# Kernel optimization log

Hardware: AMD Instinct MI355X
Metric: run time of the kernel (lower is better)

Reference implementation:

```python
import jax, jax.numpy as jnp
import numpy as np
from jax import lax


def _conv(x, w, padding):
    # NCHW input, OIHW weights, stride 1, no bias
    return lax.conv_general_dilated(x, w, (1, 1), padding,
                                    dimension_numbers=('NCHW', 'OIHW', 'NCHW'))


def setup_inputs() -> dict:
    key = jax.random.key(0)
    ks = jax.random.split(key, 6)
    B, C, H, W = 16, 512, 40, 40
    return {
        'exemplar': jax.random.normal(ks[0], (B, C, H, W), jnp.float32),
        'query':    jax.random.normal(ks[1], (B, C, H, W), jnp.float32),
        'w_e':  jax.random.normal(ks[2], (256, C, 1, 1), jnp.float32) * 0.01,
        'w_q':  jax.random.normal(ks[3], (256, C, 1, 1), jnp.float32) * 0.01,
        'w_c1': jax.random.normal(ks[4], (C, C, 3, 3), jnp.float32) * 0.01,
        'w_c2': jax.random.normal(ks[5], (C, C, 3, 3), jnp.float32) * 0.01,
    }


def reference(exemplar, query, w_e, w_q, w_c1, w_c2):
    B, C, H, W = query.shape
    N = H * W
    # 1x1 projections to 256-dim correlation space
    q_corr = _conv(query, w_q, 'VALID').reshape(B, -1, N)     # [B,256,N]
    e_corr = _conv(exemplar, w_e, 'VALID').reshape(B, -1, N)  # [B,256,N]
    # A[b, n_exemplar, m_query] = <e_corr[:, n], q_corr[:, m]>
    A = jnp.einsum('bcn,bcm->bnm', e_corr, q_corr)            # [B,N,N]
    # A1 = softmax over exemplar axis, then transpose (torch: softmax(A,dim=1).T)
    A1 = jnp.swapaxes(jax.nn.softmax(A, axis=1), 1, 2)        # [B,N,N]
    # Bm = softmax(A^T, dim=1).T  == softmax(A, axis=2)
    Bm = jnp.swapaxes(jax.nn.softmax(jnp.swapaxes(A, 1, 2), axis=1), 1, 2)
    e_flat = exemplar.reshape(B, C, N)
    q_flat = query.reshape(B, C, N)
    query_att = jnp.matmul(e_flat, A1)   # [B,C,N]
    exemplar_att = jnp.matmul(q_flat, Bm)  # [B,C,N]
    input1_att = _conv(exemplar_att.reshape(B, C, H, W), w_c1, 'SAME')
    input2_att = _conv(query_att.reshape(B, C, H, W), w_c2, 'SAME')
    return jnp.concatenate([input1_att, input2_att], axis=1)  # [B,2C,H,W]
```

## Files before the change

### kernel.cpp

```cpp
#include <hip/hip_runtime.h>

typedef unsigned short u16;
typedef __attribute__((ext_vector_type(8))) short bf16x8;
typedef __attribute__((ext_vector_type(4))) float f32x4;

__device__ __forceinline__ u16 f2bf(float f) {
  union { float f; unsigned u; } v; v.f = f;
  unsigned u = v.u;
  u += 0x7fffu + ((u >> 16) & 1u);
  return (u16)(u >> 16);
}

__device__ __forceinline__ void gll16(const void* g, void* l) {
  __builtin_amdgcn_global_load_lds(
      (const __attribute__((address_space(1))) void*)g,
      (__attribute__((address_space(3))) void*)l, 16, 0, 0);
}

__global__ __launch_bounds__(256) void transp_cast_x2(const float* __restrict__ ex,
                                                      const float* __restrict__ qu,
                                                      u16* __restrict__ xte,
                                                      u16* __restrict__ xtq) {
  __shared__ float t[32][33];
  int z = blockIdx.z;
  int b = z & 15;
  const float* xb = (z < 16 ? ex : qu) + (size_t)b * 819200;
  u16* xtb = (z < 16 ? xte : xtq) + (size_t)b * 819200;
  int n0 = blockIdx.x * 32, c0 = blockIdx.y * 32;
  int tx = threadIdx.x & 31, ty = threadIdx.x >> 5;
#pragma unroll
  for (int k = 0; k < 4; k++) {
    int c = ty + k * 8;
    t[c][tx] = xb[(size_t)(c0 + c) * 1600 + n0 + tx];
  }
  __syncthreads();
#pragma unroll
  for (int k = 0; k < 4; k++) {
    int n = ty + k * 8;
    xtb[(size_t)(n0 + n) * 512 + c0 + tx] = f2bf(t[tx][n]);
  }
}

__global__ void cast_w(const float* __restrict__ we, const float* __restrict__ wq,
                       u16* __restrict__ oe, u16* __restrict__ oq) {
  int i = blockIdx.x * 256 + threadIdx.x;
  oe[i] = f2bf(we[i]);
  oq[i] = f2bf(wq[i]);
}

__global__ void repack_wc(const float* __restrict__ w1, const float* __restrict__ w2,
                          u16* __restrict__ o1, u16* __restrict__ o2) {
  const float* w = blockIdx.y ? w2 : w1;
  u16* wr = blockIdx.y ? o2 : o1;
  int idx = blockIdx.x * 256 + threadIdx.x;
  int o = idx / 4608;
  int r = idx - o * 4608;
  int t = r >> 9;
  int c = r & 511;
  wr[idx] = f2bf(w[o * 4608 + c * 9 + t]);
}

__global__ void zero_pad(u16* __restrict__ att, float* __restrict__ Z) {
  int q = blockIdx.x;
  uint4 zz; zz.x = 0; zz.y = 0; zz.z = 0; zz.w = 0;
  if (q < 32) {
    uint4* base = (uint4*)(att + (size_t)q * 903168);
    for (int i = threadIdx.x; i < 10496; i += 256) {
      int t = i >> 6, c = i & 63;
      int y, x;
      if (t < 42) { y = 0; x = t; }
      else if (t < 84) { y = 41; x = t - 42; }
      else if (t < 124) { y = 1 + (t - 84); x = 0; }
      else { y = 1 + (t - 124); x = 41; }
      base[(y * 42 + x) * 64 + c] = zz;
    }
  } else {
    uint4* p = (uint4*)Z;
    for (int i = threadIdx.x; i < 12800; i += 256) p[i] = zz;
  }
}


__global__ __launch_bounds__(256, 2) void corr_gemm128(
    const u16* __restrict__ X1, const u16* __restrict__ Wg1, u16* __restrict__ C1,
    const u16* __restrict__ X2, const u16* __restrict__ Wg2, u16* __restrict__ C2) {
  __shared__ u16 ldsA[16384];
  __shared__ u16 ldsB[16384];
  int tid = threadIdx.x;
  int flat = blockIdx.x + blockIdx.y * 13 + blockIdx.z * 26;
  int wrk = (flat & 7) * 104 + (flat >> 3);
  int z = wrk / 26;
  int r2 = wrk - z * 26;
  int by = r2 / 13, bx = r2 - by * 13;
  int b = z & 15;
  const u16* A = (z < 16 ? X1 : X2) + (size_t)b * 819200;
  const u16* B = (z < 16 ? Wg1 : Wg2);
  u16* Cb = (z < 16 ? C1 : C2) + (size_t)b * 409600;
  int m0 = bx * 128, n0 = by * 128;

  int rl = tid >> 2;
  int cs = (tid & 3) ^ ((rl >> 1) & 3);
  int ra0 = m0 + rl; ra0 = ra0 < 1600 ? ra0 : 1599;
  int ra1 = m0 + 64 + rl; ra1 = ra1 < 1600 ? ra1 : 1599;
  const char* pA0 = (const char*)(A + (size_t)ra0 * 512) + cs * 16;
  const char* pA1 = (const char*)(A + (size_t)ra1 * 512) + cs * 16;
  const char* pB0 = (const char*)(B + (size_t)(n0 + rl) * 512) + cs * 16;
  const char* pB1 = (const char*)(B + (size_t)(n0 + 64 + rl) * 512) + cs * 16;

  char* ldsAb = (char*)ldsA;
  char* ldsBb = (char*)ldsB;
  int dstT = tid * 16;

#define STAGE_U(d, kh, ks)                                              \
  {                                                                     \
    int ko = (ks) * 64;                                                 \
    int ro = ((d) * 2 + (kh)) * 8192;                                   \
    gll16(pA0 + ko, ldsAb + ro + dstT);                                 \
    gll16(pA1 + ko, ldsAb + ro + 4096 + dstT);                          \
    gll16(pB0 + ko, ldsBb + ro + dstT);                                 \
    gll16(pB1 + ko, ldsBb + ro + 4096 + dstT);                          \
  }

  int wid = tid >> 6, lane = tid & 63;
  int wm = wid & 1, wn = wid >> 1;
  int lrow = lane & 15, lquad = lane >> 4;
  int csel = (lquad ^ ((lrow >> 1) & 3)) << 4;
  int aBase = (wm * 64 + lrow) * 64 + csel;
  int bBase = (wn * 64 + lrow) * 64 + csel;

  const f32x4 fzero = {0.f, 0.f, 0.f, 0.f};
  f32x4 acc[4][4];
#pragma unroll
  for (int mi = 0; mi < 4; mi++)
#pragma unroll
    for (int ni = 0; ni < 4; ni++) acc[mi][ni] = fzero;

  bf16x8 fa0, fa1, fa2, fa3, fb0, fb1, fb2, fb3;
  bf16x8 ga0, ga1, ga2, ga3, gb0, gb1, gb2, gb3;

#define RD(pre, d, kh)                                                  \
  {                                                                     \
    const char* ra_ = ldsAb + ((d) * 2 + (kh)) * 8192 + aBase;          \
    const char* rb_ = ldsBb + ((d) * 2 + (kh)) * 8192 + bBase;          \
    pre##a0 = *(const bf16x8*)(ra_);                                    \
    pre##a1 = *(const bf16x8*)(ra_ + 1024);                             \
    pre##a2 = *(const bf16x8*)(ra_ + 2048);                             \
    pre##a3 = *(const bf16x8*)(ra_ + 3072);                             \
    pre##b0 = *(const bf16x8*)(rb_);                                    \
    pre##b1 = *(const bf16x8*)(rb_ + 1024);                             \
    pre##b2 = *(const bf16x8*)(rb_ + 2048);                             \
    pre##b3 = *(const bf16x8*)(rb_ + 3072);                             \
  }

#define MROW(mi, av, pre)                                                               \
  acc[mi][0] = __builtin_amdgcn_mfma_f32_16x16x32_bf16(av, pre##b0, acc[mi][0], 0, 0, 0); \
  acc[mi][1] = __builtin_amdgcn_mfma_f32_16x16x32_bf16(av, pre##b1, acc[mi][1], 0, 0, 0); \
  acc[mi][2] = __builtin_amdgcn_mfma_f32_16x16x32_bf16(av, pre##b2, acc[mi][2], 0, 0, 0); \
  acc[mi][3] = __builtin_amdgcn_mfma_f32_16x16x32_bf16(av, pre##b3, acc[mi][3], 0, 0, 0);

#define MALL(pre)                                                              \
  MROW(0, pre##a0, pre) MROW(1, pre##a1, pre) MROW(2, pre##a2, pre) MROW(3, pre##a3, pre)

#define PHASE(rd_d, rd_kh, rdp, cp, STG)                                       \
  {                                                                            \
    STG;                                                                       \
    asm volatile("s_waitcnt vmcnt(4)" ::: "memory");                           \
    __builtin_amdgcn_s_barrier();                                              \
    RD(rdp, rd_d, rd_kh);                                                      \
    __builtin_amdgcn_s_setprio(1);                                             \
    MALL(cp)                                                                   \
    __builtin_amdgcn_s_setprio(0);                                             \
  }

  STAGE_U(0, 0, 0);
  STAGE_U(0, 1, 1);
  asm volatile("s_waitcnt vmcnt(4)" ::: "memory");
  __builtin_amdgcn_s_barrier();
  RD(f, 0, 0);

#pragma unroll 1
  for (int it = 0; it < 4; ++it) {
    int k2 = it * 4 + 2, k3 = it * 4 + 3;
    int k4 = it * 4 + 4; k4 = k4 < 16 ? k4 : 15;
    int k5 = it * 4 + 5; k5 = k5 < 16 ? k5 : 15;
    PHASE(0, 1, g, f, STAGE_U(1, 0, k2));
    PHASE(1, 0, f, g, STAGE_U(1, 1, k3));
    PHASE(1, 1, g, f, STAGE_U(0, 0, k4));
    PHASE(0, 0, f, g, STAGE_U(0, 1, k5));
  }

#undef PHASE
#undef MALL
#undef MROW
#undef RD
#undef STAGE_U

#pragma unroll
  for (int mi = 0; mi < 4; mi++) {
#pragma unroll
    for (int r = 0; r < 4; r++) {
      int i = m0 + wm * 64 + mi * 16 + lquad * 4 + r;
      if (i >= 1600) continue;
#pragma unroll
      for (int ni = 0; ni < 4; ni++) {
        int j = n0 + wn * 64 + ni * 16 + lrow;
        Cb[(size_t)i * 256 + j] = f2bf(acc[mi][ni][r]);
      }
    }
  }
}

__global__ __launch_bounds__(256, 2) void corr_exp128(
    const u16* __restrict__ A, const u16* __restrict__ B, u16* __restrict__ E,
    u16* __restrict__ ET, float* __restrict__ Zrow, float* __restrict__ Zcol) {
  __shared__ u16 ldsA[16384];
  __shared__ u16 ldsB[16384];
  int tid = threadIdx.x;
  int flat = blockIdx.x + blockIdx.y * 13 + blockIdx.z * 169;
  int wrk = (flat & 7) * 338 + (flat >> 3);
  int b = wrk / 169;
  int r2 = wrk - b * 169;
  int by = r2 / 13, bx = r2 - by * 13;
  const u16* Ab = A + (size_t)b * 409600;
  const u16* Bb = B + (size_t)b * 409600;
  u16* Eb = E + (size_t)b * 2560000;
  u16* ETb = ET + (size_t)b * 2560000;
  int m0 = bx * 128, n0 = by * 128;

  int rl = tid >> 2;
  int cs = (tid & 3) ^ ((rl >> 1) & 3);
  int ra0 = m0 + rl; ra0 = ra0 < 1600 ? ra0 : 1599;
  int ra1 = m0 + 64 + rl; ra1 = ra1 < 1600 ? ra1 : 1599;
  int rb0 = n0 + rl; rb0 = rb0 < 1600 ? rb0 : 1599;
  int rb1 = n0 + 64 + rl; rb1 = rb1 < 1600 ? rb1 : 1599;
  const char* pA0 = (const char*)(Ab + (size_t)ra0 * 256) + cs * 16;
  const char* pA1 = (const char*)(Ab + (size_t)ra1 * 256) + cs * 16;
  const char* pB0 = (const char*)(Bb + (size_t)rb0 * 256) + cs * 16;
  const char* pB1 = (const char*)(Bb + (size_t)rb1 * 256) + cs * 16;

  char* ldsAb = (char*)ldsA;
  char* ldsBb = (char*)ldsB;
  int dstT = tid * 16;

#define STAGE_U(d, kh, ks)                                              \
  {                                                                     \
    int ko = (ks) * 64;                                                 \
    int ro = ((d) * 2 + (kh)) * 8192;                                   \
    gll16(pA0 + ko, ldsAb + ro + dstT);                                 \
    gll16(pA1 + ko, ldsAb + ro + 4096 + dstT);                          \
    gll16(pB0 + ko, ldsBb + ro + dstT);                                 \
    gll16(pB1 + ko, ldsBb + ro + 4096 + dstT);                          \
  }

  int wid = tid >> 6, lane = tid & 63;
  int wm = wid & 1, wn = wid >> 1;
  int lrow = lane & 15, lquad = lane >> 4;
  int csel = (lquad ^ ((lrow >> 1) & 3)) << 4;
  int aBase = (wm * 64 + lrow) * 64 + csel;
  int bBase = (wn * 64 + lrow) * 64 + csel;

  const f32x4 fzero = {0.f, 0.f, 0.f, 0.f};
  f32x4 acc[4][4];
#pragma unroll
  for (int mi = 0; mi < 4; mi++)
#pragma unroll
    for (int ni = 0; ni < 4; ni++) acc[mi][ni] = fzero;

  bf16x8 fa0, fa1, fa2, fa3, fb0, fb1, fb2, fb3;
  bf16x8 ga0, ga1, ga2, ga3, gb0, gb1, gb2, gb3;

#define RD(pre, d, kh)                                                  \
  {                                                                     \
    const char* ra_ = ldsAb + ((d) * 2 + (kh)) * 8192 + aBase;          \
    const char* rb_ = ldsBb + ((d) * 2 + (kh)) * 8192 + bBase;          \
    pre##a0 = *(const bf16x8*)(ra_);                                    \
    pre##a1 = *(const bf16x8*)(ra_ + 1024);                             \
    pre##a2 = *(const bf16x8*)(ra_ + 2048);                             \
    pre##a3 = *(const bf16x8*)(ra_ + 3072);                             \
    pre##b0 = *(const bf16x8*)(rb_);                                    \
    pre##b1 = *(const bf16x8*)(rb_ + 1024);                             \
    pre##b2 = *(const bf16x8*)(rb_ + 2048);                             \
    pre##b3 = *(const bf16x8*)(rb_ + 3072);                             \
  }

#define MROW(mi, av, pre)                                                               \
  acc[mi][0] = __builtin_amdgcn_mfma_f32_16x16x32_bf16(av, pre##b0, acc[mi][0], 0, 0, 0); \
  acc[mi][1] = __builtin_amdgcn_mfma_f32_16x16x32_bf16(av, pre##b1, acc[mi][1], 0, 0, 0); \
  acc[mi][2] = __builtin_amdgcn_mfma_f32_16x16x32_bf16(av, pre##b2, acc[mi][2], 0, 0, 0); \
  acc[mi][3] = __builtin_amdgcn_mfma_f32_16x16x32_bf16(av, pre##b3, acc[mi][3], 0, 0, 0);

#define MALL(pre)                                                              \
  MROW(0, pre##a0, pre) MROW(1, pre##a1, pre) MROW(2, pre##a2, pre) MROW(3, pre##a3, pre)

#define PHASE(rd_d, rd_kh, rdp, cp, STG)                                       \
  {                                                                            \
    STG;                                                                       \
    asm volatile("s_waitcnt vmcnt(4)" ::: "memory");                           \
    __builtin_amdgcn_s_barrier();                                              \
    RD(rdp, rd_d, rd_kh);                                                      \
    __builtin_amdgcn_s_setprio(1);                                             \
    MALL(cp)                                                                   \
    __builtin_amdgcn_s_setprio(0);                                             \
  }

  STAGE_U(0, 0, 0);
  STAGE_U(0, 1, 1);
  asm volatile("s_waitcnt vmcnt(4)" ::: "memory");
  __builtin_amdgcn_s_barrier();
  RD(f, 0, 0);

#pragma unroll 1
  for (int it = 0; it < 2; ++it) {
    int k2 = it * 4 + 2, k3 = it * 4 + 3;
    int k4 = it * 4 + 4; k4 = k4 < 8 ? k4 : 7;
    int k5 = it * 4 + 5; k5 = k5 < 8 ? k5 : 7;
    PHASE(0, 1, g, f, STAGE_U(1, 0, k2));
    PHASE(1, 0, f, g, STAGE_U(1, 1, k3));
    PHASE(1, 1, g, f, STAGE_U(0, 0, k4));
    PHASE(0, 0, f, g, STAGE_U(0, 1, k5));
  }

#undef PHASE
#undef MALL
#undef MROW
#undef RD
#undef STAGE_U

  __syncthreads();

  const int TS = 136;
  u16* T = ldsA;
  float colacc[4] = {0.f, 0.f, 0.f, 0.f};
#pragma unroll
  for (int s = 0; s < 4; s++) {
    if (wm == (s >> 1)) {
      int smi0 = (s & 1) * 2;
#pragma unroll
      for (int mi2 = 0; mi2 < 2; mi2++) {
        int mi = smi0 + mi2;
        float rowp[4] = {0.f, 0.f, 0.f, 0.f};
#pragma unroll
        for (int ni = 0; ni < 4; ni++) {
          int j = n0 + wn * 64 + ni * 16 + lrow;
          bool jv = j < 1600;
#pragma unroll
          for (int r = 0; r < 4; r++) {
            int i = m0 + wm * 64 + mi * 16 + lquad * 4 + r;
            float e = __expf(acc[mi][ni][r]);
            T[(mi2 * 16 + lquad * 4 + r) * TS + wn * 64 + ni * 16 + lrow] = f2bf(e);
            rowp[r] += jv ? e : 0.f;
            colacc[ni] += (i < 1600) ? e : 0.f;
          }
        }
#pragma unroll
        for (int r = 0; r < 4; r++) {
          float v = rowp[r];
          v += __shfl_xor(v, 1);
          v += __shfl_xor(v, 2);
          v += __shfl_xor(v, 4);
          v += __shfl_xor(v, 8);
          int i = m0 + wm * 64 + mi * 16 + lquad * 4 + r;
          if (lrow == 0 && i < 1600) atomicAdd(&Zrow[b * 1600 + i], v);
        }
      }
    }
    __syncthreads();
#pragma unroll
    for (int p = 0; p < 2; p++) {
      int jj = tid + p * 256;
      int ml = jj >> 4, n8 = jj & 15;
      int gi = m0 + s * 32 + ml, gj = n0 + n8 * 8;
      if (gi < 1600 && gj < 1600)
        *(uint4*)(Eb + (size_t)gi * 1600 + gj) = *(const uint4*)&T[ml * TS + n8 * 8];
    }
#pragma unroll
    for (int p = 0; p < 4; p++) {
      int jj = tid + p * 256;
      int n = jj >> 3, m4 = jj & 7;
      int gm = m0 + s * 32 + m4 * 4, gn = n0 + n;
      if (gn < 1600 && gm < 1600) {
        ushort4 v;
        v.x = T[(m4 * 4 + 0) * TS + n];
        v.y = T[(m4 * 4 + 1) * TS + n];
        v.z = T[(m4 * 4 + 2) * TS + n];
        v.w = T[(m4 * 4 + 3) * TS + n];
        *(ushort4*)(ETb + (size_t)gn * 1600 + gm) = v;
      }
    }
    __syncthreads();
  }
#pragma unroll
  for (int ni = 0; ni < 4; ni++) {
    float v = colacc[ni];
    v += __shfl_xor(v, 16);
    v += __shfl_xor(v, 32);
    int j = n0 + wn * 64 + ni * 16 + lrow;
    if (lquad == 0 && j < 1600) atomicAdd(&Zcol[b * 1600 + j], v);
  }
}

__global__ void scale_div(const float* __restrict__ ex, const float* __restrict__ qu,
                          const float* __restrict__ Zcol, const float* __restrict__ Zrow,
                          u16* __restrict__ ebf, u16* __restrict__ qbf) {
  const float* x; const float* Z; u16* o;
  if (blockIdx.y == 0) { x = ex; Z = Zcol; o = ebf; }
  else { x = qu; Z = Zrow; o = qbf; }
  size_t idx = (size_t)blockIdx.x * 256 + threadIdx.x;
  int b = (int)(idx / 819200);
  int i = (int)(idx % 1600);
  o[idx] = f2bf(x[idx] / Z[b * 1600 + i]);
}

__global__ __launch_bounds__(256, 2) void att_gemm128(
    const u16* __restrict__ Aw1, const u16* __restrict__ Bp1, u16* __restrict__ C1,
    const u16* __restrict__ Aw2, const u16* __restrict__ Bp2, u16* __restrict__ C2) {
  __shared__ u16 ldsA[16384];
  __shared__ u16 ldsB[16384];
  int tid = threadIdx.x;
  int flat = blockIdx.x + blockIdx.y * 13 + blockIdx.z * 52;
  int wrk = (flat & 7) * 208 + (flat >> 3);
  int z = wrk / 52;
  int r2 = wrk - z * 52;
  int by = r2 / 13, bx = r2 - by * 13;
  int b = z & 15;
  const u16* Aw = (z < 16 ? Aw1 : Aw2) + (size_t)b * 819200;
  const u16* Bp = (z < 16 ? Bp1 : Bp2) + (size_t)b * 2560000;
  u16* Cb = (z < 16 ? C1 : C2) + (size_t)b * 903168;
  int p0 = bx * 128, c0 = by * 128;

  int rl = tid >> 2;
  int cs = (tid & 3) ^ ((rl >> 1) & 3);
  const char* pA0 = (const char*)(Aw + (size_t)(c0 + rl) * 1600) + cs * 16;
  const char* pA1 = pA0 + 64 * 3200;
  int pp0 = p0 + rl; pp0 = pp0 < 1600 ? pp0 : 1599;
  const char* pB0 = (const char*)(Bp + (size_t)pp0 * 1600) + cs * 16;
  int pp1 = p0 + 64 + rl; pp1 = pp1 < 1600 ? pp1 : 1599;
  const char* pB1 = (const char*)(Bp + (size_t)pp1 * 1600) + cs * 16;

  char* ldsAb = (char*)ldsA;
  char* ldsBb = (char*)ldsB;
  int dstT = tid * 16;

#define STAGE_U(d, kh, ks)                                              \
  {                                                                     \
    int ko = (ks) * 64;                                                 \
    int ro = ((d) * 2 + (kh)) * 8192;                                   \
    gll16(pA0 + ko, ldsAb + ro + dstT);                                 \
    gll16(pA1 + ko, ldsAb + ro + 4096 + dstT);                          \
    gll16(pB0 + ko, ldsBb + ro + dstT);                                 \
    gll16(pB1 + ko, ldsBb + ro + 4096 + dstT);                          \
  }

  int wid = tid >> 6, lane = tid & 63;
  int wm = wid & 1, wn = wid >> 1;
  int lrow = lane & 15, lquad = lane >> 4;
  int csel = (lquad ^ ((lrow >> 1) & 3)) << 4;
  int aBase = (wm * 64 + lrow) * 64 + csel;
  int bBase = (wn * 64 + lrow) * 64 + csel;

  const f32x4 fzero = {0.f, 0.f, 0.f, 0.f};
  f32x4 acc[4][4];
#pragma unroll
  for (int mi = 0; mi < 4; mi++)
#pragma unroll
    for (int ni = 0; ni < 4; ni++) acc[mi][ni] = fzero;

  bf16x8 fa0, fa1, fa2, fa3, fb0, fb1, fb2, fb3;
  bf16x8 ga0, ga1, ga2, ga3, gb0, gb1, gb2, gb3;

#define RD(pre, d, kh)                                                  \
  {                                                                     \
    const char* ra_ = ldsAb + ((d) * 2 + (kh)) * 8192 + aBase;          \
    const char* rb_ = ldsBb + ((d) * 2 + (kh)) * 8192 + bBase;          \
    pre##a0 = *(const bf16x8*)(ra_);                                    \
    pre##a1 = *(const bf16x8*)(ra_ + 1024);                             \
    pre##a2 = *(const bf16x8*)(ra_ + 2048);                             \
    pre##a3 = *(const bf16x8*)(ra_ + 3072);                             \
    pre##b0 = *(const bf16x8*)(rb_);                                    \
    pre##b1 = *(const bf16x8*)(rb_ + 1024);                             \
    pre##b2 = *(const bf16x8*)(rb_ + 2048);                             \
    pre##b3 = *(const bf16x8*)(rb_ + 3072);                             \
  }

#define MROW(mi, av, pre)                                                               \
  acc[mi][0] = __builtin_amdgcn_mfma_f32_16x16x32_bf16(av, pre##b0, acc[mi][0], 0, 0, 0); \
  acc[mi][1] = __builtin_amdgcn_mfma_f32_16x16x32_bf16(av, pre##b1, acc[mi][1], 0, 0, 0); \
  acc[mi][2] = __builtin_amdgcn_mfma_f32_16x16x32_bf16(av, pre##b2, acc[mi][2], 0, 0, 0); \
  acc[mi][3] = __builtin_amdgcn_mfma_f32_16x16x32_bf16(av, pre##b3, acc[mi][3], 0, 0, 0);

#define MALL(pre)                                                              \
  MROW(0, pre##a0, pre) MROW(1, pre##a1, pre) MROW(2, pre##a2, pre) MROW(3, pre##a3, pre)

#define PHASE(rd_d, rd_kh, rdp, cp, STG)                                       \
  {                                                                            \
    STG;                                                                       \
    asm volatile("s_waitcnt vmcnt(4)" ::: "memory");                           \
    __builtin_amdgcn_s_barrier();                                              \
    RD(rdp, rd_d, rd_kh);                                                      \
    __builtin_amdgcn_s_setprio(1);                                             \
    MALL(cp)                                                                   \
    __builtin_amdgcn_s_setprio(0);                                             \
  }

  STAGE_U(0, 0, 0);
  STAGE_U(0, 1, 1);
  asm volatile("s_waitcnt vmcnt(4)" ::: "memory");
  __builtin_amdgcn_s_barrier();
  RD(f, 0, 0);

#pragma unroll 1
  for (int it = 0; it < 12; ++it) {
    int k2 = it * 4 + 2, k3 = it * 4 + 3, k4 = it * 4 + 4, k5 = it * 4 + 5;
    PHASE(0, 1, g, f, STAGE_U(1, 0, k2));
    PHASE(1, 0, f, g, STAGE_U(1, 1, k3));
    PHASE(1, 1, g, f, STAGE_U(0, 0, k4));
    PHASE(0, 0, f, g, STAGE_U(0, 1, k5));
  }
  asm volatile("s_waitcnt vmcnt(0)" ::: "memory");
  __builtin_amdgcn_s_barrier();
  RD(g, 0, 1);
  __builtin_amdgcn_s_setprio(1);
  MALL(f)
  MALL(g)
  __builtin_amdgcn_s_setprio(0);

#undef PHASE
#undef MALL
#undef MROW
#undef RD
#undef STAGE_U

#pragma unroll
  for (int mi = 0; mi < 4; mi++) {
#pragma unroll
    for (int r = 0; r < 4; r++) {
      int o = c0 + wm * 64 + mi * 16 + lquad * 4 + r;
#pragma unroll
      for (int ni = 0; ni < 4; ni++) {
        int p = p0 + wn * 64 + ni * 16 + lrow;
        if (p < 1600) {
          int y = p / 40, x = p - y * 40;
          Cb[(size_t)((y + 1) * 42 + (x + 1)) * 512 + o] = f2bf(acc[mi][ni][r]);
        }
      }
    }
  }
}

__global__ __launch_bounds__(512, 2) void conv_gemmpf(
    const u16* __restrict__ W1, const u16* __restrict__ ATT1,
    const u16* __restrict__ W2, const u16* __restrict__ ATT2,
    float* __restrict__ out) {
  __shared__ u16 ldsA[32768];
  __shared__ u16 ldsB[32768];
  int tid = threadIdx.x;
  int z = blockIdx.z, b = z & 15, sel2 = z >> 4;
  const u16* W = sel2 ? W2 : W1;
  const u16* attb = (sel2 ? ATT2 : ATT1) + (size_t)b * 903168;
  float* outb = out + (size_t)b * 1638400 + (size_t)(sel2 ? 512 : 0) * 1600;
  int p0 = blockIdx.x * 224, o0 = blockIdx.y * 256;

  int rl = tid >> 2;
  int cs = (tid & 3) ^ ((rl >> 1) & 3);
  const char* pA0 = (const char*)(W + (size_t)(o0 + rl) * 4608) + cs * 16;
  const char* pA1 = pA0 + 128 * 9216;
  int pp0 = p0 + rl; pp0 = pp0 < 1600 ? pp0 : 1599;
  int y0 = pp0 / 40, x0 = pp0 - y0 * 40;
  const char* pB0 = (const char*)(attb + (size_t)(y0 * 42 + x0) * 512) + cs * 16;
  int pp1 = p0 + 128 + rl; pp1 = pp1 < 1600 ? pp1 : 1599;
  int y1 = pp1 / 40, x1 = pp1 - y1 * 40;
  const char* pB1 = (const char*)(attb + (size_t)(y1 * 42 + x1) * 512) + cs * 16;

  char* ldsAb = (char*)ldsA;
  char* ldsBb = (char*)ldsB;
  int dstT = tid * 16;

#define STAGE_A(d, kh, kt)                                              \
  {                                                                     \
    int ko = (kt) * 128 + (kh) * 64;                                    \
    gll16(pA0 + ko, ldsAb + ((d) * 2 + (kh)) * 16384 + dstT);           \
    gll16(pA1 + ko, ldsAb + ((d) * 2 + (kh)) * 16384 + 8192 + dstT);    \
  }
#define STAGE_B(d, kh, kt)                                              \
  {                                                                     \
    int tp = (kt) >> 3;                                                 \
    int ty = (tp * 11) >> 5;                                            \
    int tx = tp - ty * 3;                                               \
    int ko = (ty * 42 + tx) * 1024 + ((kt) & 7) * 128 + (kh) * 64;      \
    gll16(pB0 + ko, ldsBb + ((d) * 2 + (kh)) * 16384 + dstT);           \
    gll16(pB1 + ko, ldsBb + ((d) * 2 + (kh)) * 16384 + 8192 + dstT);    \
  }
#define STAGE_U(d, kh, kt) { STAGE_A(d, kh, kt); STAGE_B(d, kh, kt); }

  int wid = tid >> 6, lane = tid & 63;
  int wm = wid & 3, wn = wid >> 2;
  int lrow = lane & 15, lquad = lane >> 4;
  int csel = (lquad ^ ((lrow >> 1) & 3)) << 4;
  int aBase = (wm * 64 + lrow) * 64 + csel;
  int bBase = (wn * 112 + lrow) * 64 + csel;

  const f32x4 fzero = {0.f, 0.f, 0.f, 0.f};
  f32x4 acc[4][7];
#pragma unroll
  for (int mi = 0; mi < 4; mi++)
#pragma unroll
    for (int ni = 0; ni < 7; ni++) acc[mi][ni] = fzero;

  bf16x8 fa0, fa1, fa2, fa3, fb0, fb1, fb2, fb3, fb4, fb5, fb6;
  bf16x8 ga0, ga1, ga2, ga3, gb0, gb1, gb2, gb3, gb4, gb5, gb6;

#define RD(pre, d, kh)                                                  \
  {                                                                     \
    const char* ra_ = ldsAb + ((d) * 2 + (kh)) * 16384 + aBase;         \
    const char* rb_ = ldsBb + ((d) * 2 + (kh)) * 16384 + bBase;         \
    pre##a0 = *(const bf16x8*)(ra_);                                    \
    pre##a1 = *(const bf16x8*)(ra_ + 1024);                             \
    pre##a2 = *(const bf16x8*)(ra_ + 2048);                             \
    pre##a3 = *(const bf16x8*)(ra_ + 3072);                             \
    pre##b0 = *(const bf16x8*)(rb_);                                    \
    pre##b1 = *(const bf16x8*)(rb_ + 1024);                             \
    pre##b2 = *(const bf16x8*)(rb_ + 2048);                             \
    pre##b3 = *(const bf16x8*)(rb_ + 3072);                             \
    pre##b4 = *(const bf16x8*)(rb_ + 4096);                             \
    pre##b5 = *(const bf16x8*)(rb_ + 5120);                             \
    pre##b6 = *(const bf16x8*)(rb_ + 6144);                             \
  }

#define MROW(mi, av, pre)                                                               \
  acc[mi][0] = __builtin_amdgcn_mfma_f32_16x16x32_bf16(av, pre##b0, acc[mi][0], 0, 0, 0); \
  acc[mi][1] = __builtin_amdgcn_mfma_f32_16x16x32_bf16(av, pre##b1, acc[mi][1], 0, 0, 0); \
  acc[mi][2] = __builtin_amdgcn_mfma_f32_16x16x32_bf16(av, pre##b2, acc[mi][2], 0, 0, 0); \
  acc[mi][3] = __builtin_amdgcn_mfma_f32_16x16x32_bf16(av, pre##b3, acc[mi][3], 0, 0, 0); \
  acc[mi][4] = __builtin_amdgcn_mfma_f32_16x16x32_bf16(av, pre##b4, acc[mi][4], 0, 0, 0); \
  acc[mi][5] = __builtin_amdgcn_mfma_f32_16x16x32_bf16(av, pre##b5, acc[mi][5], 0, 0, 0); \
  acc[mi][6] = __builtin_amdgcn_mfma_f32_16x16x32_bf16(av, pre##b6, acc[mi][6], 0, 0, 0);

#define PHASE(rd_d, rd_kh, rdp, cp, STG)                                       \
  {                                                                            \
    STG;                                                                       \
    asm volatile("s_waitcnt vmcnt(4)" ::: "memory");                           \
    __builtin_amdgcn_s_barrier();                                              \
    RD(rdp, rd_d, rd_kh);                                                      \
    __builtin_amdgcn_s_setprio(1);                                             \
    MROW(0, cp##a0, cp)                                                        \
    MROW(1, cp##a1, cp)                                                        \
    MROW(2, cp##a2, cp)                                                        \
    MROW(3, cp##a3, cp)                                                        \
    __builtin_amdgcn_s_setprio(0);                                             \
  }

  STAGE_U(0, 0, 0);
  STAGE_U(0, 1, 0);
  asm volatile("s_waitcnt vmcnt(4)" ::: "memory");
  __builtin_amdgcn_s_barrier();
  RD(f, 0, 0);

#pragma unroll 1
  for (int it = 0; it < 36; ++it) {
    int kt1 = it * 2 + 1;
    int kt2 = it < 35 ? it * 2 + 2 : 71;
    PHASE(0, 1, g, f, STAGE_U(1, 0, kt1));
    PHASE(1, 0, f, g, STAGE_U(1, 1, kt1));
    PHASE(1, 1, g, f, STAGE_U(0, 0, kt2));
    PHASE(0, 0, f, g, STAGE_U(0, 1, kt2));
  }

#undef PHASE
#undef MROW
#undef RD
#undef STAGE_U
#undef STAGE_A
#undef STAGE_B

#pragma unroll
  for (int mi = 0; mi < 4; mi++) {
#pragma unroll
    for (int r = 0; r < 4; r++) {
      int o = o0 + wm * 64 + mi * 16 + lquad * 4 + r;
      float* orow = outb + (size_t)o * 1600;
#pragma unroll
      for (int ni = 0; ni < 7; ni++) {
        int p = p0 + wn * 112 + ni * 16 + lrow;
        if (p < 1600) orow[p] = acc[mi][ni][r];
      }
    }
  }
}

extern "C" void kernel_launch(void* const* d_in, const int* in_sizes, int n_in,
                              void* d_out, int out_size, void* d_ws, size_t ws_size,
                              hipStream_t stream) {
  const float* ex = (const float*)d_in[0];
  const float* qu = (const float*)d_in[1];
  const float* w_e = (const float*)d_in[2];
  const float* w_q = (const float*)d_in[3];
  const float* w_c1 = (const float*)d_in[4];
  const float* w_c2 = (const float*)d_in[5];
  float* out = (float*)d_out;
  char* ws = (char*)d_ws;

  u16* E     = (u16*)(ws + 0L);
  u16* ET    = (u16*)(ws + 81920000L);
  u16* xt_e  = (u16*)(ws + 163840000L);
  u16* xt_q  = (u16*)(ws + 190054400L);
  u16* ecorr = (u16*)(ws + 216268800L);
  u16* qcorr = (u16*)(ws + 229376000L);
  u16* att_e = (u16*)(ws + 242483200L);
  u16* att_q = (u16*)(ws + 271384576L);
  float* Zrow = (float*)(ws + 300285952L);
  float* Zcol = (float*)(ws + 300388352L);
  u16* w_ebf = (u16*)(ws + 300490752L);
  u16* w_qbf = (u16*)(ws + 300752896L);
  u16* wr1   = (u16*)(ws + 301015040L);
  u16* wr2   = (u16*)(ws + 305733632L);

  transp_cast_x2<<<dim3(50, 16, 32), 256, 0, stream>>>(ex, qu, xt_e, xt_q);
  cast_w<<<dim3(512), 256, 0, stream>>>(w_e, w_q, w_ebf, w_qbf);
  repack_wc<<<dim3(9216, 2), 256, 0, stream>>>(w_c1, w_c2, wr1, wr2);
  zero_pad<<<dim3(33), 256, 0, stream>>>(att_e, Zrow);

  corr_gemm128<<<dim3(13, 2, 32), 256, 0, stream>>>(
      xt_e, w_ebf, ecorr, xt_q, w_qbf, qcorr);

  corr_exp128<<<dim3(13, 13, 16), 256, 0, stream>>>(ecorr, qcorr, E, ET, Zrow, Zcol);

  u16* ebf = xt_e;
  u16* qbf = xt_q;
  scale_div<<<dim3(51200, 2), 256, 0, stream>>>(ex, qu, Zcol, Zrow, ebf, qbf);

  att_gemm128<<<dim3(13, 4, 32), 256, 0, stream>>>(ebf, E, att_q, qbf, ET, att_e);

  conv_gemmpf<<<dim3(8, 2, 32), 512, 0, stream>>>(wr1, att_e, wr2, att_q, out);
}
```

Measured before the change: 796.1 us.

## Fuse softmax normalization and bf16 cast into attention GEMM A-operand loads

Removes the separate scale_div pass, which read the fp32 inputs and wrote bf16 copies divided by the softmax denominators. The attention GEMM now loads fp32 activations directly into registers, multiplies by precomputed reciprocal denominators, packs them to bf16 with v_cvt_pk_bf16_f32 and writes them to LDS after the MFMA block. A small inv_z kernel turns the sums into reciprocals, and the conv GEMM block index gets remapped with an XCD-style swizzle. In exchange the GEMM reads twice as many bytes for A and does register staging with an extra lgkmcnt wait per phase.

```diff
diff --git a/kernel.cpp b/kernel.cpp
--- a/kernel.cpp
+++ b/kernel.cpp
@@ -9,6 +9,12 @@
   unsigned u = v.u;
   u += 0x7fffu + ((u >> 16) & 1u);
   return (u16)(u >> 16);
+}
+
+__device__ __forceinline__ unsigned pk2(float lo, float hi) {
+  unsigned r;
+  asm("v_cvt_pk_bf16_f32 %0, %1, %2" : "=v"(r) : "v"(lo), "v"(hi));
+  return r;
 }
 
 __device__ __forceinline__ void gll16(const void* g, void* l) {
@@ -80,6 +86,11 @@
   }
 }
 
+__global__ void inv_z(float* __restrict__ Z) {
+  int i = blockIdx.x * 256 + threadIdx.x;
+  Z[i] = 1.0f / Z[i];
+}
+
 
 __global__ __launch_bounds__(256, 2) void corr_gemm128(
     const u16* __restrict__ X1, const u16* __restrict__ Wg1, u16* __restrict__ C1,
@@ -399,21 +410,11 @@
   }
 }
 
-__global__ void scale_div(const float* __restrict__ ex, const float* __restrict__ qu,
-                          const float* __restrict__ Zcol, const float* __restrict__ Zrow,
-                          u16* __restrict__ ebf, u16* __restrict__ qbf) {
-  const float* x; const float* Z; u16* o;
-  if (blockIdx.y == 0) { x = ex; Z = Zcol; o = ebf; }
-  else { x = qu; Z = Zrow; o = qbf; }
-  size_t idx = (size_t)blockIdx.x * 256 + threadIdx.x;
-  int b = (int)(idx / 819200);
-  int i = (int)(idx % 1600);
-  o[idx] = f2bf(x[idx] / Z[b * 1600 + i]);
-}
-
-__global__ __launch_bounds__(256, 2) void att_gemm128(
-    const u16* __restrict__ Aw1, const u16* __restrict__ Bp1, u16* __restrict__ C1,
-    const u16* __restrict__ Aw2, const u16* __restrict__ Bp2, u16* __restrict__ C2) {
+__global__ __launch_bounds__(256, 2) void att_fuse128(
+    const float* __restrict__ Xe, const float* __restrict__ Xq,
+    const float* __restrict__ iZc, const float* __restrict__ iZr,
+    const u16* __restrict__ E, const u16* __restrict__ ET,
+    u16* __restrict__ Cq, u16* __restrict__ Ce) {
   __shared__ u16 ldsA[16384];
   __shared__ u16 ldsB[16384];
   int tid = threadIdx.x;
@@ -423,15 +424,17 @@
   int r2 = wrk - z * 52;
   int by = r2 / 13, bx = r2 - by * 13;
   int b = z & 15;
-  const u16* Aw = (z < 16 ? Aw1 : Aw2) + (size_t)b * 819200;
-  const u16* Bp = (z < 16 ? Bp1 : Bp2) + (size_t)b * 2560000;
-  u16* Cb = (z < 16 ? C1 : C2) + (size_t)b * 903168;
+  const float* X = (z < 16 ? Xe : Xq) + (size_t)b * 819200;
+  const float* iZ = (z < 16 ? iZc : iZr) + b * 1600;
+  const u16* Bp = (z < 16 ? E : ET) + (size_t)b * 2560000;
+  u16* Cb = (z < 16 ? Cq : Ce) + (size_t)b * 903168;
   int p0 = bx * 128, c0 = by * 128;
 
   int rl = tid >> 2;
   int cs = (tid & 3) ^ ((rl >> 1) & 3);
-  const char* pA0 = (const char*)(Aw + (size_t)(c0 + rl) * 1600) + cs * 16;
-  const char* pA1 = pA0 + 64 * 3200;
+  const float* pX0 = X + (size_t)(c0 + rl) * 1600 + cs * 8;
+  const float* pX1 = pX0 + (size_t)64 * 1600;
+  const float* pZ = iZ + cs * 8;
   int pp0 = p0 + rl; pp0 = pp0 < 1600 ? pp0 : 1599;
   const char* pB0 = (const char*)(Bp + (size_t)pp0 * 1600) + cs * 16;
   int pp1 = p0 + 64 + rl; pp1 = pp1 < 1600 ? pp1 : 1599;
@@ -441,14 +444,38 @@
   char* ldsBb = (char*)ldsB;
   int dstT = tid * 16;
 
-#define STAGE_U(d, kh, ks)                                              \
+  float4 a00, a01, a10, a11, zz0, zz1;
+
+#define ALD(ks)                                                         \
+  a00 = *(const float4*)(pX0 + (ks) * 32);                              \
+  a01 = *(const float4*)(pX0 + (ks) * 32 + 4);                          \
+  a10 = *(const float4*)(pX1 + (ks) * 32);                              \
+  a11 = *(const float4*)(pX1 + (ks) * 32 + 4);                          \
+  zz0 = *(const float4*)(pZ + (ks) * 32);                               \
+  zz1 = *(const float4*)(pZ + (ks) * 32 + 4);
+
+#define BST(d, kh, ks)                                                  \
   {                                                                     \
     int ko = (ks) * 64;                                                 \
     int ro = ((d) * 2 + (kh)) * 8192;                                   \
-    gll16(pA0 + ko, ldsAb + ro + dstT);                                 \
-    gll16(pA1 + ko, ldsAb + ro + 4096 + dstT);                          \
     gll16(pB0 + ko, ldsBb + ro + dstT);                                 \
     gll16(pB1 + ko, ldsBb + ro + 4096 + dstT);                          \
+  }
+
+#define AWR(d, kh)                                                      \
+  {                                                                     \
+    int ro = ((d) * 2 + (kh)) * 8192;                                   \
+    uint4 w0, w1;                                                       \
+    w0.x = pk2(a00.x * zz0.x, a00.y * zz0.y);                           \
+    w0.y = pk2(a00.z * zz0.z, a00.w * zz0.w);                           \
+    w0.z = pk2(a01.x * zz1.x, a01.y * zz1.y);                           \
+    w0.w = pk2(a01.z * zz1.z, a01.w * zz1.w);                           \
+    w1.x = pk2(a10.x * zz0.x, a10.y * zz0.y);                           \
+    w1.y = pk2(a10.z * zz0.z, a10.w * zz0.w);                           \
+    w1.z = pk2(a11.x * zz1.x, a11.y * zz1.y);                           \
+    w1.w = pk2(a11.z * zz1.z, a11.w * zz1.w);                           \
+    *(uint4*)(ldsAb + ro + dstT) = w0;                                  \
+    *(uint4*)(ldsAb + ro + 4096 + dstT) = w1;                           \
   }
 
   int wid = tid >> 6, lane = tid & 63;
@@ -491,30 +518,34 @@
 #define MALL(pre)                                                              \
   MROW(0, pre##a0, pre) MROW(1, pre##a1, pre) MROW(2, pre##a2, pre) MROW(3, pre##a3, pre)
 
-#define PHASE(rd_d, rd_kh, rdp, cp, STG)                                       \
+#define PHASE(rd_d, rd_kh, rdp, cp, st_d, st_kh, st_ks)                        \
   {                                                                            \
-    STG;                                                                       \
-    asm volatile("s_waitcnt vmcnt(4)" ::: "memory");                           \
+    ALD(st_ks);                                                                \
+    BST(st_d, st_kh, st_ks);                                                   \
+    asm volatile("s_waitcnt vmcnt(8)" ::: "memory");                           \
     __builtin_amdgcn_s_barrier();                                              \
     RD(rdp, rd_d, rd_kh);                                                      \
     __builtin_amdgcn_s_setprio(1);                                             \
     MALL(cp)                                                                   \
     __builtin_amdgcn_s_setprio(0);                                             \
-  }
-
-  STAGE_U(0, 0, 0);
-  STAGE_U(0, 1, 1);
-  asm volatile("s_waitcnt vmcnt(4)" ::: "memory");
+    AWR(st_d, st_kh);                                                          \
+    asm volatile("s_waitcnt lgkmcnt(0)" ::: "memory");                         \
+  }
+
+  ALD(0); BST(0, 0, 0); AWR(0, 0);
+  ALD(1); BST(0, 1, 1); AWR(0, 1);
+  asm volatile("s_waitcnt vmcnt(0)" ::: "memory");
+  asm volatile("s_waitcnt lgkmcnt(0)" ::: "memory");
   __builtin_amdgcn_s_barrier();
   RD(f, 0, 0);
 
 #pragma unroll 1
   for (int it = 0; it < 12; ++it) {
     int k2 = it * 4 + 2, k3 = it * 4 + 3, k4 = it * 4 + 4, k5 = it * 4 + 5;
-    PHASE(0, 1, g, f, STAGE_U(1, 0, k2));
-    PHASE(1, 0, f, g, STAGE_U(1, 1, k3));
-    PHASE(1, 1, g, f, STAGE_U(0, 0, k4));
-    PHASE(0, 0, f, g, STAGE_U(0, 1, k5));
+    PHASE(0, 1, g, f, 1, 0, k2);
+    PHASE(1, 0, f, g, 1, 1, k3);
+    PHASE(1, 1, g, f, 0, 0, k4);
+    PHASE(0, 0, f, g, 0, 1, k5);
   }
   asm volatile("s_waitcnt vmcnt(0)" ::: "memory");
   __builtin_amdgcn_s_barrier();
@@ -528,7 +559,9 @@
 #undef MALL
 #undef MROW
 #undef RD
-#undef STAGE_U
+#undef AWR
+#undef BST
+#undef ALD
 
 #pragma unroll
   for (int mi = 0; mi < 4; mi++) {
@@ -554,11 +587,16 @@
   __shared__ u16 ldsA[32768];
   __shared__ u16 ldsB[32768];
   int tid = threadIdx.x;
-  int z = blockIdx.z, b = z & 15, sel2 = z >> 4;
+  int h = blockIdx.x + blockIdx.y * 8 + blockIdx.z * 16;
+  int wrk = (h & 7) * 64 + (h >> 3);
+  int by = wrk & 1;
+  int q = wrk >> 1;
+  int bx = q & 7, z = q >> 3;
+  int b = z & 15, sel2 = z >> 4;
   const u16* W = sel2 ? W2 : W1;
   const u16* attb = (sel2 ? ATT2 : ATT1) + (size_t)b * 903168;
   float* outb = out + (size_t)b * 1638400 + (size_t)(sel2 ? 512 : 0) * 1600;
-  int p0 = blockIdx.x * 224, o0 = blockIdx.y * 256;
+  int p0 = bx * 224, o0 = by * 256;
 
   int rl = tid >> 2;
   int cs = (tid & 3) ^ ((rl >> 1) & 3);
@@ -724,11 +762,10 @@
 
   corr_exp128<<<dim3(13, 13, 16), 256, 0, stream>>>(ecorr, qcorr, E, ET, Zrow, Zcol);
 
-  u16* ebf = xt_e;
-  u16* qbf = xt_q;
-  scale_div<<<dim3(51200, 2), 256, 0, stream>>>(ex, qu, Zcol, Zrow, ebf, qbf);
-
-  att_gemm128<<<dim3(13, 4, 32), 256, 0, stream>>>(ebf, E, att_q, qbf, ET, att_e);
+  inv_z<<<dim3(200), 256, 0, stream>>>(Zrow);
+
+  att_fuse128<<<dim3(13, 4, 32), 256, 0, stream>>>(
+      ex, qu, Zcol, Zrow, E, ET, att_q, att_e);
 
   conv_gemmpf<<<dim3(8, 2, 32), 512, 0, stream>>>(wr1, att_e, wr2, att_q, out);
 }
```

After: 789.4 us. About the same (-0.8%).
